# Kernel optimization log

Hardware: AMD Instinct MI355X
Metric: run time of the kernel (lower is better)

Reference implementation:

```python
import jax, jax.numpy as jnp
import numpy as np

B, N, D, M, C = 4, 256, 128, 128, 128


def _lin_init(key, din, dout):
    # torch nn.Linear default: U(-1/sqrt(din), 1/sqrt(din)) for weight and bias
    bound = 1.0 / np.sqrt(din)
    kw, kb = jax.random.split(key)
    W = jax.random.uniform(kw, (din, dout), jnp.float32, -bound, bound)
    b = jax.random.uniform(kb, (dout,), jnp.float32, -bound, bound)
    return W, b


def setup_inputs() -> dict:
    key = jax.random.key(0)
    k_h, k_adj, k1, k2, k3, k4 = jax.random.split(key, 6)
    h = jax.random.normal(k_h, (B, N, D), jnp.float32)
    adj = jax.random.uniform(k_adj, (B, N, N), jnp.float32)
    # msg MLP: Linear(2D -> M), SiLU, Linear(M -> M). Split first weight into
    # the h_i block (W1a) and h_j block (W1b) of the concatenated input.
    W1, b1 = _lin_init(k1, 2 * D, M)
    W1a, W1b = W1[:D], W1[D:]
    W2, b2 = _lin_init(k2, M, M)
    # to_c MLP: Linear(M -> M), SiLU, Linear(M -> C)
    Wc1, bc1 = _lin_init(k3, M, M)
    Wc2, bc2 = _lin_init(k4, M, C)
    return {"h": h, "adj": adj, "W1a": W1a, "W1b": W1b, "b1": b1,
            "W2": W2, "b2": b2, "Wc1": Wc1, "bc1": bc1, "Wc2": Wc2, "bc2": bc2}


def reference(h, adj, W1a, W1b, b1, W2, b2, Wc1, bc1, Wc2, bc2):
    n = h.shape[1]
    # First msg Linear on cat([h_i, h_j]) == h_i @ W1a + h_j @ W1b + b1.
    # Precompute per-node projections once instead of the (B,N,N,2D) pair tensor.
    pi = jnp.einsum('bnd,dm->bnm', h, W1a)           # (B,N,M) for destination i
    pj = jnp.einsum('bnd,dm->bnm', h, W1b)           # (B,N,M) for source j
    pre = pi[:, :, None, :] + pj[:, None, :, :] + b1  # (B,N,N,M)
    m = jnp.einsum('bijm,mk->bijk', jax.nn.silu(pre), W2) + b2  # (B,N,N,M)
    # zero self-messages (diagonal ignored), then weight by adjacency
    mask = (1.0 - jnp.eye(n, dtype=h.dtype))[None, :, :, None]
    m = m * mask * adj[..., None]
    # mean aggregation over source nodes j with clamped degree
    denom = jnp.clip(jnp.sum(adj, axis=-1, keepdims=True), 1.0)  # (B,N,1)
    m_agg = jnp.sum(m, axis=2) / denom                           # (B,N,M)
    c = jnp.einsum('bnm,mc->bnc', jax.nn.silu(jnp.einsum('bnm,mk->bnk', m_agg, Wc1) + bc1), Wc2) + bc2
    return c
```

## Files before the change

### kernel.cpp

```cpp
#include <hip/hip_runtime.h>
#include <math.h>

#define BB 4
#define NN 256
#define DD 128
#define MM 128
#define CC 128
#define ROWS (BB * NN)

static __device__ __forceinline__ float fast_exp2(float x) {
#if __has_builtin(__builtin_amdgcn_exp2f)
    return __builtin_amdgcn_exp2f(x);
#else
    return __exp2f(x);
#endif
}

static __device__ __forceinline__ float fast_rcp(float x) {
#if __has_builtin(__builtin_amdgcn_rcpf)
    return __builtin_amdgcn_rcpf(x);
#else
    return 1.0f / x;
#endif
}

static __device__ __forceinline__ float silu_f(float x) {
    float e = fast_exp2(-1.44269504088896340736f * x);
    return x * fast_rcp(1.0f + e);
}

template <int R>
__global__ __launch_bounds__(256) void k_proj(const float* __restrict__ h,
                                              const float* __restrict__ W1a,
                                              const float* __restrict__ W1b,
                                              const float* __restrict__ b1,
                                              float* __restrict__ pibias,
                                              float* __restrict__ pj) {
    __shared__ float sWa[32 * MM];
    __shared__ float sWb[32 * MM];
    __shared__ float sH[R * DD];

    const int t = threadIdx.x;
    const int m = t & 127;
    const int rh = t >> 7;
    const int row0 = blockIdx.x * R;

    const float bias = b1[m];

    const float* hbase = h + (size_t)row0 * DD;
    sH[t] = hbase[t];
    sH[t + 256] = hbase[t + 256];

    float accA[2] = {0.0f, 0.0f};
    float accB[2] = {0.0f, 0.0f};

    for (int c = 0; c < 4; ++c) {
        __syncthreads();
        const float4* ga = (const float4*)(W1a + (size_t)c * 32 * MM);
        const float4* gb = (const float4*)(W1b + (size_t)c * 32 * MM);
        float4* la = (float4*)sWa;
        float4* lb = (float4*)sWb;
        #pragma unroll
        for (int i = 0; i < 4; ++i) {
            la[t + 256 * i] = ga[t + 256 * i];
            lb[t + 256 * i] = gb[t + 256 * i];
        }
        __syncthreads();

        #pragma unroll 8
        for (int dd = 0; dd < 32; ++dd) {
            const int d = c * 32 + dd;
            const float wa = sWa[dd * MM + m];
            const float wb = sWb[dd * MM + m];
            #pragma unroll
            for (int r = 0; r < 2; ++r) {
                const float hv = sH[(rh * 2 + r) * DD + d];
                accA[r] = fmaf(hv, wa, accA[r]);
                accB[r] = fmaf(hv, wb, accB[r]);
            }
        }
    }

    #pragma unroll
    for (int r = 0; r < 2; ++r) {
        const int row = row0 + rh * 2 + r;
        pibias[(size_t)row * MM + m] = accA[r] + bias;
        pj[(size_t)row * MM + m]     = accB[r];
    }
}

__global__ __launch_bounds__(256) void k_msg(const float* __restrict__ adj,
                                             const float* __restrict__ pibias,
                                             const float* __restrict__ pj,
                                             float* __restrict__ S,
                                             float* __restrict__ beta) {
    __shared__ float sPJ[64 * MM];
    __shared__ float sAdj[2][NN];
    __shared__ float sRed[2][256];
    __shared__ float sWred[2][4];

    const int t = threadIdx.x;
    const int pairIdx = blockIdx.x;
    const int b = pairIdx >> 7;
    const int i0 = (pairIdx & 127) * 2;
    const int row0 = b * NN + i0;

    const int m = t & 127;
    const int jh = t >> 7;

    const float* arow = adj + (size_t)row0 * NN;
    const float a0v = arow[t];
    const float a1v = arow[t + 256];
    const float pim0 = pibias[(size_t)row0 * MM + m];
    const float pim1 = pibias[(size_t)(row0 + 1) * MM + m];

    sAdj[0][t] = a0v;
    sAdj[1][t] = a1v;
    __syncthreads();

    float v0 = a0v, v1 = a1v;
    #pragma unroll
    for (int off = 32; off > 0; off >>= 1) {
        v0 += __shfl_xor(v0, off, 64);
        v1 += __shfl_xor(v1, off, 64);
    }
    if ((t & 63) == 0) { sWred[0][t >> 6] = v0; sWred[1][t >> 6] = v1; }
    __syncthreads();
    const float A0 = sWred[0][0] + sWred[0][1] + sWred[0][2] + sWred[0][3];
    const float A1 = sWred[1][0] + sWred[1][1] + sWred[1][2] + sWred[1][3];
    const float aii0 = sAdj[0][i0];
    const float aii1 = sAdj[1][i0 + 1];
    __syncthreads();
    if (t == 0) { sAdj[0][i0] = 0.0f; sAdj[1][i0 + 1] = 0.0f; }

    const float inv0 = 1.0f / fmaxf(A0, 1.0f);
    const float inv1 = 1.0f / fmaxf(A1, 1.0f);

    const float* __restrict__ pjB = pj + (size_t)b * NN * MM;

    float acc0 = 0.0f, acc1 = 0.0f;
    for (int c = 0; c < 4; ++c) {
        __syncthreads();
        const float4* g = (const float4*)(pjB + (size_t)c * 64 * MM);
        float4* l = (float4*)sPJ;
        #pragma unroll
        for (int i = 0; i < 8; ++i) l[t + 256 * i] = g[t + 256 * i];
        __syncthreads();

        #pragma unroll 8
        for (int jj = jh; jj < 64; jj += 2) {
            const int j = c * 64 + jj;
            const float pjv = sPJ[jj * MM + m];
            const float w0 = sAdj[0][j];
            const float w1 = sAdj[1][j];
            acc0 = fmaf(w0, silu_f(pim0 + pjv), acc0);
            acc1 = fmaf(w1, silu_f(pim1 + pjv), acc1);
        }
    }

    sRed[0][t] = acc0;
    sRed[1][t] = acc1;
    __syncthreads();
    if (t < 128) {
        S[(size_t)row0 * MM + t] = (sRed[0][t] + sRed[0][t + 128]) * inv0;
    } else {
        const int k = t - 128;
        S[(size_t)(row0 + 1) * MM + k] = (sRed[1][k] + sRed[1][k + 128]) * inv1;
    }
    if (t == 0) {
        beta[row0]     = (A0 - aii0) * inv0;
        beta[row0 + 1] = (A1 - aii1) * inv1;
    }
}

__device__ __forceinline__ void matvec_staged(const float* __restrict__ W,
                                              const float* __restrict__ src,
                                              float* __restrict__ sW,
                                              float acc[2], int t, int k, int rh) {
    for (int c = 0; c < 2; ++c) {
        __syncthreads();
        const float4* g = (const float4*)(W + (size_t)c * 64 * MM);
        float4* l = (float4*)sW;
        #pragma unroll
        for (int i = 0; i < 8; ++i) l[t + 256 * i] = g[t + 256 * i];
        __syncthreads();

        #pragma unroll 8
        for (int dd = 0; dd < 64; ++dd) {
            const int d = c * 64 + dd;
            const float wv = sW[dd * MM + k];
            acc[0] = fmaf(src[(rh * 2 + 0) * MM + d], wv, acc[0]);
            acc[1] = fmaf(src[(rh * 2 + 1) * MM + d], wv, acc[1]);
        }
    }
}

template <int R>
__global__ __launch_bounds__(256) void k_out(const float* __restrict__ S,
                                             const float* __restrict__ beta,
                                             const float* __restrict__ W2,
                                             const float* __restrict__ b2,
                                             const float* __restrict__ Wc1,
                                             const float* __restrict__ bc1,
                                             const float* __restrict__ Wc2,
                                             const float* __restrict__ bc2,
                                             float* __restrict__ out) {
    __shared__ float sW[64 * MM];
    __shared__ float sA[R * MM];
    __shared__ float sB[R * MM];

    const int t = threadIdx.x;
    const int k = t & 127;
    const int rh = t >> 7;
    const int row0 = blockIdx.x * R;

    const float bet0 = beta[row0 + rh * 2];
    const float bet1 = beta[row0 + rh * 2 + 1];
    const float b2k  = b2[k];
    const float bc1k = bc1[k];
    const float bc2k = bc2[k];

    const float* sbase = S + (size_t)row0 * MM;
    sA[t] = sbase[t];
    sA[t + 256] = sbase[t + 256];

    float acc[2];

    acc[0] = bet0 * b2k;
    acc[1] = bet1 * b2k;
    matvec_staged(W2, sA, sW, acc, t, k, rh);
    sB[(rh * 2 + 0) * MM + k] = acc[0];
    sB[(rh * 2 + 1) * MM + k] = acc[1];

    acc[0] = bc1k;
    acc[1] = bc1k;
    matvec_staged(Wc1, sB, sW, acc, t, k, rh);
    sA[(rh * 2 + 0) * MM + k] = silu_f(acc[0]);
    sA[(rh * 2 + 1) * MM + k] = silu_f(acc[1]);

    acc[0] = bc2k;
    acc[1] = bc2k;
    matvec_staged(Wc2, sA, sW, acc, t, k, rh);
    out[(size_t)(row0 + rh * 2 + 0) * CC + k] = acc[0];
    out[(size_t)(row0 + rh * 2 + 1) * CC + k] = acc[1];
}

extern "C" void kernel_launch(void* const* d_in, const int* in_sizes, int n_in,
                              void* d_out, int out_size, void* d_ws, size_t ws_size,
                              hipStream_t stream) {
    const float* h   = (const float*)d_in[0];
    const float* adj = (const float*)d_in[1];
    const float* W1a = (const float*)d_in[2];
    const float* W1b = (const float*)d_in[3];
    const float* b1  = (const float*)d_in[4];
    const float* W2  = (const float*)d_in[5];
    const float* b2  = (const float*)d_in[6];
    const float* Wc1 = (const float*)d_in[7];
    const float* bc1 = (const float*)d_in[8];
    const float* Wc2 = (const float*)d_in[9];
    const float* bc2 = (const float*)d_in[10];
    float* out = (float*)d_out;

    float* ws = (float*)d_ws;
    float* pibias = ws;
    float* pj     = ws + (size_t)ROWS * MM;
    float* S      = ws + (size_t)2 * ROWS * MM;
    float* beta   = ws + (size_t)3 * ROWS * MM;

    k_proj<4><<<ROWS / 4, 256, 0, stream>>>(h, W1a, W1b, b1, pibias, pj);
    k_msg<<<ROWS / 2, 256, 0, stream>>>(adj, pibias, pj, S, beta);
    k_out<4><<<ROWS / 4, 256, 0, stream>>>(S, beta, W2, b2, Wc1, bc1, Wc2, bc2, out);
}
```

Baseline: 105.8 us.

## Fuse three kernels into one cooperative kernel with grid sync

Replaces the projection, message and output kernels with a single cooperative kernel of 256 blocks, each handling 4 rows. A grid-wide sync separates the projection phase from the message phase, and only pj goes through global memory. pibias, S and beta stay in shared memory. Each block now processes 4 destination rows per pj pass instead of 2, halving pj re-staging, and the final MLP matvecs split the reduction dimension across the two thread halves. In exchange there are fewer blocks (256 on a GPU with many CUs), the cost of a grid sync, and larger shared memory use, which lowers parallelism in the dominant message phase.

```diff
diff --git a/kernel.cpp b/kernel.cpp
--- a/kernel.cpp
+++ b/kernel.cpp
@@ -1,5 +1,8 @@
 #include <hip/hip_runtime.h>
+#include <hip/hip_cooperative_groups.h>
 #include <math.h>
+
+namespace cg = cooperative_groups;
 
 #define BB 4
 #define NN 256
@@ -29,154 +32,11 @@
     return x * fast_rcp(1.0f + e);
 }
 
-template <int R>
-__global__ __launch_bounds__(256) void k_proj(const float* __restrict__ h,
-                                              const float* __restrict__ W1a,
-                                              const float* __restrict__ W1b,
-                                              const float* __restrict__ b1,
-                                              float* __restrict__ pibias,
-                                              float* __restrict__ pj) {
-    __shared__ float sWa[32 * MM];
-    __shared__ float sWb[32 * MM];
-    __shared__ float sH[R * DD];
-
-    const int t = threadIdx.x;
-    const int m = t & 127;
-    const int rh = t >> 7;
-    const int row0 = blockIdx.x * R;
-
-    const float bias = b1[m];
-
-    const float* hbase = h + (size_t)row0 * DD;
-    sH[t] = hbase[t];
-    sH[t + 256] = hbase[t + 256];
-
-    float accA[2] = {0.0f, 0.0f};
-    float accB[2] = {0.0f, 0.0f};
-
-    for (int c = 0; c < 4; ++c) {
-        __syncthreads();
-        const float4* ga = (const float4*)(W1a + (size_t)c * 32 * MM);
-        const float4* gb = (const float4*)(W1b + (size_t)c * 32 * MM);
-        float4* la = (float4*)sWa;
-        float4* lb = (float4*)sWb;
-        #pragma unroll
-        for (int i = 0; i < 4; ++i) {
-            la[t + 256 * i] = ga[t + 256 * i];
-            lb[t + 256 * i] = gb[t + 256 * i];
-        }
-        __syncthreads();
-
-        #pragma unroll 8
-        for (int dd = 0; dd < 32; ++dd) {
-            const int d = c * 32 + dd;
-            const float wa = sWa[dd * MM + m];
-            const float wb = sWb[dd * MM + m];
-            #pragma unroll
-            for (int r = 0; r < 2; ++r) {
-                const float hv = sH[(rh * 2 + r) * DD + d];
-                accA[r] = fmaf(hv, wa, accA[r]);
-                accB[r] = fmaf(hv, wb, accB[r]);
-            }
-        }
-    }
-
-    #pragma unroll
-    for (int r = 0; r < 2; ++r) {
-        const int row = row0 + rh * 2 + r;
-        pibias[(size_t)row * MM + m] = accA[r] + bias;
-        pj[(size_t)row * MM + m]     = accB[r];
-    }
-}
-
-__global__ __launch_bounds__(256) void k_msg(const float* __restrict__ adj,
-                                             const float* __restrict__ pibias,
-                                             const float* __restrict__ pj,
-                                             float* __restrict__ S,
-                                             float* __restrict__ beta) {
-    __shared__ float sPJ[64 * MM];
-    __shared__ float sAdj[2][NN];
-    __shared__ float sRed[2][256];
-    __shared__ float sWred[2][4];
-
-    const int t = threadIdx.x;
-    const int pairIdx = blockIdx.x;
-    const int b = pairIdx >> 7;
-    const int i0 = (pairIdx & 127) * 2;
-    const int row0 = b * NN + i0;
-
-    const int m = t & 127;
-    const int jh = t >> 7;
-
-    const float* arow = adj + (size_t)row0 * NN;
-    const float a0v = arow[t];
-    const float a1v = arow[t + 256];
-    const float pim0 = pibias[(size_t)row0 * MM + m];
-    const float pim1 = pibias[(size_t)(row0 + 1) * MM + m];
-
-    sAdj[0][t] = a0v;
-    sAdj[1][t] = a1v;
-    __syncthreads();
-
-    float v0 = a0v, v1 = a1v;
-    #pragma unroll
-    for (int off = 32; off > 0; off >>= 1) {
-        v0 += __shfl_xor(v0, off, 64);
-        v1 += __shfl_xor(v1, off, 64);
-    }
-    if ((t & 63) == 0) { sWred[0][t >> 6] = v0; sWred[1][t >> 6] = v1; }
-    __syncthreads();
-    const float A0 = sWred[0][0] + sWred[0][1] + sWred[0][2] + sWred[0][3];
-    const float A1 = sWred[1][0] + sWred[1][1] + sWred[1][2] + sWred[1][3];
-    const float aii0 = sAdj[0][i0];
-    const float aii1 = sAdj[1][i0 + 1];
-    __syncthreads();
-    if (t == 0) { sAdj[0][i0] = 0.0f; sAdj[1][i0 + 1] = 0.0f; }
-
-    const float inv0 = 1.0f / fmaxf(A0, 1.0f);
-    const float inv1 = 1.0f / fmaxf(A1, 1.0f);
-
-    const float* __restrict__ pjB = pj + (size_t)b * NN * MM;
-
-    float acc0 = 0.0f, acc1 = 0.0f;
-    for (int c = 0; c < 4; ++c) {
-        __syncthreads();
-        const float4* g = (const float4*)(pjB + (size_t)c * 64 * MM);
-        float4* l = (float4*)sPJ;
-        #pragma unroll
-        for (int i = 0; i < 8; ++i) l[t + 256 * i] = g[t + 256 * i];
-        __syncthreads();
-
-        #pragma unroll 8
-        for (int jj = jh; jj < 64; jj += 2) {
-            const int j = c * 64 + jj;
-            const float pjv = sPJ[jj * MM + m];
-            const float w0 = sAdj[0][j];
-            const float w1 = sAdj[1][j];
-            acc0 = fmaf(w0, silu_f(pim0 + pjv), acc0);
-            acc1 = fmaf(w1, silu_f(pim1 + pjv), acc1);
-        }
-    }
-
-    sRed[0][t] = acc0;
-    sRed[1][t] = acc1;
-    __syncthreads();
-    if (t < 128) {
-        S[(size_t)row0 * MM + t] = (sRed[0][t] + sRed[0][t + 128]) * inv0;
-    } else {
-        const int k = t - 128;
-        S[(size_t)(row0 + 1) * MM + k] = (sRed[1][k] + sRed[1][k + 128]) * inv1;
-    }
-    if (t == 0) {
-        beta[row0]     = (A0 - aii0) * inv0;
-        beta[row0 + 1] = (A1 - aii1) * inv1;
-    }
-}
-
-__device__ __forceinline__ void matvec_staged(const float* __restrict__ W,
+static __device__ __forceinline__ void mat128(const float* __restrict__ W,
                                               const float* __restrict__ src,
                                               float* __restrict__ sW,
-                                              float acc[2], int t, int k, int rh) {
+                                              float* __restrict__ sP,
+                                              float acc[4], int t, int k, int half) {
     for (int c = 0; c < 2; ++c) {
         __syncthreads();
         const float4* g = (const float4*)(W + (size_t)c * 64 * MM);
@@ -185,64 +45,207 @@
         for (int i = 0; i < 8; ++i) l[t + 256 * i] = g[t + 256 * i];
         __syncthreads();
 
+        const int dd0 = half * 32;
         #pragma unroll 8
-        for (int dd = 0; dd < 64; ++dd) {
+        for (int dd = dd0; dd < dd0 + 32; ++dd) {
             const int d = c * 64 + dd;
             const float wv = sW[dd * MM + k];
-            acc[0] = fmaf(src[(rh * 2 + 0) * MM + d], wv, acc[0]);
-            acc[1] = fmaf(src[(rh * 2 + 1) * MM + d], wv, acc[1]);
-        }
-    }
-}
-
-template <int R>
-__global__ __launch_bounds__(256) void k_out(const float* __restrict__ S,
-                                             const float* __restrict__ beta,
+            #pragma unroll
+            for (int r = 0; r < 4; ++r) acc[r] = fmaf(src[r * MM + d], wv, acc[r]);
+        }
+    }
+    if (half == 1) {
+        #pragma unroll
+        for (int r = 0; r < 4; ++r) sP[r * MM + k] = acc[r];
+    }
+    __syncthreads();
+    if (half == 0) {
+        #pragma unroll
+        for (int r = 0; r < 4; ++r) acc[r] += sP[r * MM + k];
+    }
+}
+
+__global__ __launch_bounds__(256) void fused(const float* __restrict__ h,
+                                             const float* __restrict__ adj,
+                                             const float* __restrict__ W1a,
+                                             const float* __restrict__ W1b,
+                                             const float* __restrict__ b1,
                                              const float* __restrict__ W2,
                                              const float* __restrict__ b2,
                                              const float* __restrict__ Wc1,
                                              const float* __restrict__ bc1,
                                              const float* __restrict__ Wc2,
                                              const float* __restrict__ bc2,
-                                             float* __restrict__ out) {
-    __shared__ float sW[64 * MM];
-    __shared__ float sA[R * MM];
-    __shared__ float sB[R * MM];
+                                             float* __restrict__ out,
+                                             float* __restrict__ pjws) {
+    __shared__ float sStage[64 * MM];
+    __shared__ float sH[4 * DD];
+    __shared__ float sPib[4 * MM];
+    __shared__ float sAdj[4][NN];
+    __shared__ float sRed[4 * 256];
+    __shared__ float sS[4 * MM];
+    __shared__ float sB[4 * MM];
+    __shared__ float sWred[4][4];
 
     const int t = threadIdx.x;
-    const int k = t & 127;
-    const int rh = t >> 7;
-    const int row0 = blockIdx.x * R;
-
-    const float bet0 = beta[row0 + rh * 2];
-    const float bet1 = beta[row0 + rh * 2 + 1];
-    const float b2k  = b2[k];
-    const float bc1k = bc1[k];
-    const float bc2k = bc2[k];
-
-    const float* sbase = S + (size_t)row0 * MM;
-    sA[t] = sbase[t];
-    sA[t + 256] = sbase[t + 256];
-
-    float acc[2];
-
-    acc[0] = bet0 * b2k;
-    acc[1] = bet1 * b2k;
-    matvec_staged(W2, sA, sW, acc, t, k, rh);
-    sB[(rh * 2 + 0) * MM + k] = acc[0];
-    sB[(rh * 2 + 1) * MM + k] = acc[1];
-
-    acc[0] = bc1k;
-    acc[1] = bc1k;
-    matvec_staged(Wc1, sB, sW, acc, t, k, rh);
-    sA[(rh * 2 + 0) * MM + k] = silu_f(acc[0]);
-    sA[(rh * 2 + 1) * MM + k] = silu_f(acc[1]);
-
-    acc[0] = bc2k;
-    acc[1] = bc2k;
-    matvec_staged(Wc2, sA, sW, acc, t, k, rh);
-    out[(size_t)(row0 + rh * 2 + 0) * CC + k] = acc[0];
-    out[(size_t)(row0 + rh * 2 + 1) * CC + k] = acc[1];
+    const int blk = blockIdx.x;
+    const int row0 = blk * 4;
+    const int b = blk >> 6;
+    const int i0 = (blk & 63) * 4;
+
+    const int m = t & 127;
+    const int half = t >> 7;
+
+    const float b1m  = b1[m];
+    const float b2k  = b2[m];
+    const float bc1k = bc1[m];
+    const float bc2k = bc2[m];
+
+    {
+        const float* hbase = h + (size_t)row0 * DD;
+        sH[t] = hbase[t];
+        sH[t + 256] = hbase[t + 256];
+
+        float accA0 = 0.f, accA1 = 0.f, accB0 = 0.f, accB1 = 0.f;
+        for (int c = 0; c < 4; ++c) {
+            __syncthreads();
+            const float4* ga = (const float4*)(W1a + (size_t)c * 32 * MM);
+            const float4* gb = (const float4*)(W1b + (size_t)c * 32 * MM);
+            float4* la = (float4*)sStage;
+            float4* lb = (float4*)(sStage + 32 * MM);
+            #pragma unroll
+            for (int i = 0; i < 4; ++i) {
+                la[t + 256 * i] = ga[t + 256 * i];
+                lb[t + 256 * i] = gb[t + 256 * i];
+            }
+            __syncthreads();
+            #pragma unroll 8
+            for (int dd = 0; dd < 32; ++dd) {
+                const int d = c * 32 + dd;
+                const float wa = sStage[dd * MM + m];
+                const float wb = sStage[32 * MM + dd * MM + m];
+                const float h0 = sH[(half * 2 + 0) * DD + d];
+                const float h1 = sH[(half * 2 + 1) * DD + d];
+                accA0 = fmaf(h0, wa, accA0);
+                accA1 = fmaf(h1, wa, accA1);
+                accB0 = fmaf(h0, wb, accB0);
+                accB1 = fmaf(h1, wb, accB1);
+            }
+        }
+        sPib[(half * 2 + 0) * MM + m] = accA0 + b1m;
+        sPib[(half * 2 + 1) * MM + m] = accA1 + b1m;
+        float* pjrow = pjws + (size_t)(row0 + half * 2) * MM;
+        pjrow[m]      = accB0;
+        pjrow[MM + m] = accB1;
+    }
+
+    cg::this_grid().sync();
+
+    float inv[4], bet[4];
+    {
+        const float* arow = adj + (size_t)row0 * NN;
+        float* sAdjF = (float*)sAdj;
+        #pragma unroll
+        for (int i = 0; i < 4; ++i) sAdjF[t + 256 * i] = arow[t + 256 * i];
+        __syncthreads();
+
+        float v0 = sAdj[0][t], v1 = sAdj[1][t], v2 = sAdj[2][t], v3 = sAdj[3][t];
+        #pragma unroll
+        for (int off = 32; off > 0; off >>= 1) {
+            v0 += __shfl_xor(v0, off, 64);
+            v1 += __shfl_xor(v1, off, 64);
+            v2 += __shfl_xor(v2, off, 64);
+            v3 += __shfl_xor(v3, off, 64);
+        }
+        if ((t & 63) == 0) {
+            const int w = t >> 6;
+            sWred[0][w] = v0; sWred[1][w] = v1; sWred[2][w] = v2; sWred[3][w] = v3;
+        }
+        __syncthreads();
+        float A[4], aii[4];
+        #pragma unroll
+        for (int r = 0; r < 4; ++r) {
+            A[r] = sWred[r][0] + sWred[r][1] + sWred[r][2] + sWred[r][3];
+            aii[r] = sAdj[r][i0 + r];
+        }
+        __syncthreads();
+        if (t < 4) sAdj[t][i0 + t] = 0.0f;
+        #pragma unroll
+        for (int r = 0; r < 4; ++r) {
+            inv[r] = 1.0f / fmaxf(A[r], 1.0f);
+            bet[r] = (A[r] - aii[r]) * inv[r];
+        }
+
+        const float pim0 = sPib[0 * MM + m];
+        const float pim1 = sPib[1 * MM + m];
+        const float pim2 = sPib[2 * MM + m];
+        const float pim3 = sPib[3 * MM + m];
+        const float* __restrict__ pjB = pjws + (size_t)b * NN * MM;
+
+        float acc0 = 0.f, acc1 = 0.f, acc2 = 0.f, acc3 = 0.f;
+        for (int c = 0; c < 4; ++c) {
+            __syncthreads();
+            const float4* g = (const float4*)(pjB + (size_t)c * 64 * MM);
+            float4* l = (float4*)sStage;
+            #pragma unroll
+            for (int i = 0; i < 8; ++i) l[t + 256 * i] = g[t + 256 * i];
+            __syncthreads();
+
+            #pragma unroll 4
+            for (int jj = half; jj < 64; jj += 2) {
+                const int j = c * 64 + jj;
+                const float pjv = sStage[jj * MM + m];
+                const float w0 = sAdj[0][j];
+                const float w1 = sAdj[1][j];
+                const float w2 = sAdj[2][j];
+                const float w3 = sAdj[3][j];
+                acc0 = fmaf(w0, silu_f(pim0 + pjv), acc0);
+                acc1 = fmaf(w1, silu_f(pim1 + pjv), acc1);
+                acc2 = fmaf(w2, silu_f(pim2 + pjv), acc2);
+                acc3 = fmaf(w3, silu_f(pim3 + pjv), acc3);
+            }
+        }
+
+        sRed[0 * 256 + t] = acc0;
+        sRed[1 * 256 + t] = acc1;
+        sRed[2 * 256 + t] = acc2;
+        sRed[3 * 256 + t] = acc3;
+        __syncthreads();
+        if (t < 128) {
+            #pragma unroll
+            for (int r = 0; r < 4; ++r)
+                sS[r * MM + t] = (sRed[r * 256 + t] + sRed[r * 256 + t + 128]) * inv[r];
+        }
+    }
+
+    {
+        float acc[4];
+
+        #pragma unroll
+        for (int r = 0; r < 4; ++r) acc[r] = (half == 0) ? bet[r] * b2k : 0.0f;
+        mat128(W2, sS, sStage, sRed, acc, t, m, half);
+        if (half == 0) {
+            #pragma unroll
+            for (int r = 0; r < 4; ++r) sB[r * MM + m] = acc[r];
+        }
+
+        #pragma unroll
+        for (int r = 0; r < 4; ++r) acc[r] = (half == 0) ? bc1k : 0.0f;
+        mat128(Wc1, sB, sStage, sRed, acc, t, m, half);
+        if (half == 0) {
+            #pragma unroll
+            for (int r = 0; r < 4; ++r) sS[r * MM + m] = silu_f(acc[r]);
+        }
+
+        #pragma unroll
+        for (int r = 0; r < 4; ++r) acc[r] = (half == 0) ? bc2k : 0.0f;
+        mat128(Wc2, sS, sStage, sRed, acc, t, m, half);
+        if (half == 0) {
+            #pragma unroll
+            for (int r = 0; r < 4; ++r)
+                out[(size_t)(row0 + r) * CC + m] = acc[r];
+        }
+    }
 }
 
 extern "C" void kernel_launch(void* const* d_in, const int* in_sizes, int n_in,
@@ -260,14 +263,11 @@
     const float* Wc2 = (const float*)d_in[9];
     const float* bc2 = (const float*)d_in[10];
     float* out = (float*)d_out;
-
-    float* ws = (float*)d_ws;
-    float* pibias = ws;
-    float* pj     = ws + (size_t)ROWS * MM;
-    float* S      = ws + (size_t)2 * ROWS * MM;
-    float* beta   = ws + (size_t)3 * ROWS * MM;
-
-    k_proj<4><<<ROWS / 4, 256, 0, stream>>>(h, W1a, W1b, b1, pibias, pj);
-    k_msg<<<ROWS / 2, 256, 0, stream>>>(adj, pibias, pj, S, beta);
-    k_out<4><<<ROWS / 4, 256, 0, stream>>>(S, beta, W2, b2, Wc1, bc1, Wc2, bc2, out);
-}
+    float* pjws = (float*)d_ws;
+
+    void* args[] = {(void*)&h, (void*)&adj, (void*)&W1a, (void*)&W1b, (void*)&b1,
+                    (void*)&W2, (void*)&b2, (void*)&Wc1, (void*)&bc1,
+                    (void*)&Wc2, (void*)&bc2, (void*)&out, (void*)&pjws};
+    hipLaunchCooperativeKernel(reinterpret_cast<void*>(fused),
+                               dim3(256), dim3(256), args, 0, stream);
+}
```

After: 150.3 us. +42.1%, slower.

## Fuse message aggregation and output MLP into one kernel, shrink projection tiles

Applied to the files above, without the earlier changes.

Merges the message-aggregation kernel with the output MLP kernel so S and beta stay in shared memory instead of going through global memory, and removes one launch. The projection kernel now handles 2 rows per block instead of 4. In exchange, each block stages W2, Wc1 and Wc2 for only two rows, doubling weight reloads from L2 across the grid.

```diff
diff --git a/kernel.cpp b/kernel.cpp
--- a/kernel.cpp
+++ b/kernel.cpp
@@ -29,7 +29,6 @@
     return x * fast_rcp(1.0f + e);
 }
 
-template <int R>
 __global__ __launch_bounds__(256) void k_proj(const float* __restrict__ h,
                                               const float* __restrict__ W1a,
                                               const float* __restrict__ W1b,
@@ -38,22 +37,18 @@
                                               float* __restrict__ pj) {
     __shared__ float sWa[32 * MM];
     __shared__ float sWb[32 * MM];
-    __shared__ float sH[R * DD];
+    __shared__ float sH[2 * DD];
 
     const int t = threadIdx.x;
     const int m = t & 127;
-    const int rh = t >> 7;
-    const int row0 = blockIdx.x * R;
+    const int r = t >> 7;
+    const int row0 = blockIdx.x * 2;
 
     const float bias = b1[m];
 
-    const float* hbase = h + (size_t)row0 * DD;
-    sH[t] = hbase[t];
-    sH[t + 256] = hbase[t + 256];
-
-    float accA[2] = {0.0f, 0.0f};
-    float accB[2] = {0.0f, 0.0f};
-
+    sH[t] = h[(size_t)row0 * DD + t];
+
+    float accA = 0.0f, accB = 0.0f;
     for (int c = 0; c < 4; ++c) {
         __syncthreads();
         const float4* ga = (const float4*)(W1a + (size_t)c * 32 * MM);
@@ -70,50 +65,52 @@
         #pragma unroll 8
         for (int dd = 0; dd < 32; ++dd) {
             const int d = c * 32 + dd;
-            const float wa = sWa[dd * MM + m];
-            const float wb = sWb[dd * MM + m];
-            #pragma unroll
-            for (int r = 0; r < 2; ++r) {
-                const float hv = sH[(rh * 2 + r) * DD + d];
-                accA[r] = fmaf(hv, wa, accA[r]);
-                accB[r] = fmaf(hv, wb, accB[r]);
-            }
-        }
-    }
-
-    #pragma unroll
-    for (int r = 0; r < 2; ++r) {
-        const int row = row0 + rh * 2 + r;
-        pibias[(size_t)row * MM + m] = accA[r] + bias;
-        pj[(size_t)row * MM + m]     = accB[r];
-    }
-}
-
-__global__ __launch_bounds__(256) void k_msg(const float* __restrict__ adj,
-                                             const float* __restrict__ pibias,
-                                             const float* __restrict__ pj,
-                                             float* __restrict__ S,
-                                             float* __restrict__ beta) {
-    __shared__ float sPJ[64 * MM];
+            const float hv = sH[r * DD + d];
+            accA = fmaf(hv, sWa[dd * MM + m], accA);
+            accB = fmaf(hv, sWb[dd * MM + m], accB);
+        }
+    }
+
+    const int row = row0 + r;
+    pibias[(size_t)row * MM + m] = accA + bias;
+    pj[(size_t)row * MM + m]     = accB;
+}
+
+__global__ __launch_bounds__(256) void k_msgout(const float* __restrict__ adj,
+                                                const float* __restrict__ pibias,
+                                                const float* __restrict__ pj,
+                                                const float* __restrict__ W2,
+                                                const float* __restrict__ b2,
+                                                const float* __restrict__ Wc1,
+                                                const float* __restrict__ bc1,
+                                                const float* __restrict__ Wc2,
+                                                const float* __restrict__ bc2,
+                                                float* __restrict__ out) {
+    __shared__ float sStage[64 * MM];
     __shared__ float sAdj[2][NN];
     __shared__ float sRed[2][256];
+    __shared__ float sS[2 * MM];
+    __shared__ float sB[2 * MM];
     __shared__ float sWred[2][4];
 
     const int t = threadIdx.x;
-    const int pairIdx = blockIdx.x;
-    const int b = pairIdx >> 7;
-    const int i0 = (pairIdx & 127) * 2;
+    const int blk = blockIdx.x;
+    const int b = blk >> 7;
+    const int i0 = (blk & 127) * 2;
     const int row0 = b * NN + i0;
 
     const int m = t & 127;
-    const int jh = t >> 7;
+    const int half = t >> 7;
+
+    const float b2k  = b2[m];
+    const float bc1k = bc1[m];
+    const float bc2k = bc2[m];
+    const float pim0 = pibias[(size_t)row0 * MM + m];
+    const float pim1 = pibias[(size_t)(row0 + 1) * MM + m];
 
     const float* arow = adj + (size_t)row0 * NN;
     const float a0v = arow[t];
     const float a1v = arow[t + 256];
-    const float pim0 = pibias[(size_t)row0 * MM + m];
-    const float pim1 = pibias[(size_t)(row0 + 1) * MM + m];
-
     sAdj[0][t] = a0v;
     sAdj[1][t] = a1v;
     __syncthreads();
@@ -135,22 +132,23 @@
 
     const float inv0 = 1.0f / fmaxf(A0, 1.0f);
     const float inv1 = 1.0f / fmaxf(A1, 1.0f);
+    const float bet0 = (A0 - aii0) * inv0;
+    const float bet1 = (A1 - aii1) * inv1;
 
     const float* __restrict__ pjB = pj + (size_t)b * NN * MM;
-
     float acc0 = 0.0f, acc1 = 0.0f;
     for (int c = 0; c < 4; ++c) {
         __syncthreads();
         const float4* g = (const float4*)(pjB + (size_t)c * 64 * MM);
-        float4* l = (float4*)sPJ;
-        #pragma unroll
-        for (int i = 0; i < 8; ++i) l[t + 256 * i] = g[t + 256 * i];
-        __syncthreads();
-
-        #pragma unroll 8
-        for (int jj = jh; jj < 64; jj += 2) {
+        float4* l = (float4*)sStage;
+        #pragma unroll
+        for (int i = 0; i < 8; ++i) l[t + 256 * i] = g[t + 256 * i];
+        __syncthreads();
+
+        #pragma unroll 8
+        for (int jj = half; jj < 64; jj += 2) {
             const int j = c * 64 + jj;
-            const float pjv = sPJ[jj * MM + m];
+            const float pjv = sStage[jj * MM + m];
             const float w0 = sAdj[0][j];
             const float w1 = sAdj[1][j];
             acc0 = fmaf(w0, silu_f(pim0 + pjv), acc0);
@@ -162,87 +160,62 @@
     sRed[1][t] = acc1;
     __syncthreads();
     if (t < 128) {
-        S[(size_t)row0 * MM + t] = (sRed[0][t] + sRed[0][t + 128]) * inv0;
+        sS[t] = (sRed[0][t] + sRed[0][t + 128]) * inv0;
     } else {
         const int k = t - 128;
-        S[(size_t)(row0 + 1) * MM + k] = (sRed[1][k] + sRed[1][k + 128]) * inv1;
-    }
-    if (t == 0) {
-        beta[row0]     = (A0 - aii0) * inv0;
-        beta[row0 + 1] = (A1 - aii1) * inv1;
-    }
-}
-
-__device__ __forceinline__ void matvec_staged(const float* __restrict__ W,
-                                              const float* __restrict__ src,
-                                              float* __restrict__ sW,
-                                              float acc[2], int t, int k, int rh) {
+        sS[MM + k] = (sRed[1][k] + sRed[1][k + 128]) * inv1;
+    }
+
+    const float betr = (half == 0) ? bet0 : bet1;
+
+    float acc = betr * b2k;
     for (int c = 0; c < 2; ++c) {
         __syncthreads();
-        const float4* g = (const float4*)(W + (size_t)c * 64 * MM);
-        float4* l = (float4*)sW;
-        #pragma unroll
-        for (int i = 0; i < 8; ++i) l[t + 256 * i] = g[t + 256 * i];
-        __syncthreads();
-
+        const float4* g = (const float4*)(W2 + (size_t)c * 64 * MM);
+        float4* l = (float4*)sStage;
+        #pragma unroll
+        for (int i = 0; i < 8; ++i) l[t + 256 * i] = g[t + 256 * i];
+        __syncthreads();
         #pragma unroll 8
         for (int dd = 0; dd < 64; ++dd) {
             const int d = c * 64 + dd;
-            const float wv = sW[dd * MM + k];
-            acc[0] = fmaf(src[(rh * 2 + 0) * MM + d], wv, acc[0]);
-            acc[1] = fmaf(src[(rh * 2 + 1) * MM + d], wv, acc[1]);
-        }
-    }
-}
-
-template <int R>
-__global__ __launch_bounds__(256) void k_out(const float* __restrict__ S,
-                                             const float* __restrict__ beta,
-                                             const float* __restrict__ W2,
-                                             const float* __restrict__ b2,
-                                             const float* __restrict__ Wc1,
-                                             const float* __restrict__ bc1,
-                                             const float* __restrict__ Wc2,
-                                             const float* __restrict__ bc2,
-                                             float* __restrict__ out) {
-    __shared__ float sW[64 * MM];
-    __shared__ float sA[R * MM];
-    __shared__ float sB[R * MM];
-
-    const int t = threadIdx.x;
-    const int k = t & 127;
-    const int rh = t >> 7;
-    const int row0 = blockIdx.x * R;
-
-    const float bet0 = beta[row0 + rh * 2];
-    const float bet1 = beta[row0 + rh * 2 + 1];
-    const float b2k  = b2[k];
-    const float bc1k = bc1[k];
-    const float bc2k = bc2[k];
-
-    const float* sbase = S + (size_t)row0 * MM;
-    sA[t] = sbase[t];
-    sA[t + 256] = sbase[t + 256];
-
-    float acc[2];
-
-    acc[0] = bet0 * b2k;
-    acc[1] = bet1 * b2k;
-    matvec_staged(W2, sA, sW, acc, t, k, rh);
-    sB[(rh * 2 + 0) * MM + k] = acc[0];
-    sB[(rh * 2 + 1) * MM + k] = acc[1];
-
-    acc[0] = bc1k;
-    acc[1] = bc1k;
-    matvec_staged(Wc1, sB, sW, acc, t, k, rh);
-    sA[(rh * 2 + 0) * MM + k] = silu_f(acc[0]);
-    sA[(rh * 2 + 1) * MM + k] = silu_f(acc[1]);
-
-    acc[0] = bc2k;
-    acc[1] = bc2k;
-    matvec_staged(Wc2, sA, sW, acc, t, k, rh);
-    out[(size_t)(row0 + rh * 2 + 0) * CC + k] = acc[0];
-    out[(size_t)(row0 + rh * 2 + 1) * CC + k] = acc[1];
+            acc = fmaf(sS[half * MM + d], sStage[dd * MM + m], acc);
+        }
+    }
+    sB[half * MM + m] = acc;
+
+    acc = bc1k;
+    for (int c = 0; c < 2; ++c) {
+        __syncthreads();
+        const float4* g = (const float4*)(Wc1 + (size_t)c * 64 * MM);
+        float4* l = (float4*)sStage;
+        #pragma unroll
+        for (int i = 0; i < 8; ++i) l[t + 256 * i] = g[t + 256 * i];
+        __syncthreads();
+        #pragma unroll 8
+        for (int dd = 0; dd < 64; ++dd) {
+            const int d = c * 64 + dd;
+            acc = fmaf(sB[half * MM + d], sStage[dd * MM + m], acc);
+        }
+    }
+    __syncthreads();
+    sS[half * MM + m] = silu_f(acc);
+
+    acc = bc2k;
+    for (int c = 0; c < 2; ++c) {
+        __syncthreads();
+        const float4* g = (const float4*)(Wc2 + (size_t)c * 64 * MM);
+        float4* l = (float4*)sStage;
+        #pragma unroll
+        for (int i = 0; i < 8; ++i) l[t + 256 * i] = g[t + 256 * i];
+        __syncthreads();
+        #pragma unroll 8
+        for (int dd = 0; dd < 64; ++dd) {
+            const int d = c * 64 + dd;
+            acc = fmaf(sS[half * MM + d], sStage[dd * MM + m], acc);
+        }
+    }
+    out[(size_t)(row0 + half) * CC + m] = acc;
 }
 
 extern "C" void kernel_launch(void* const* d_in, const int* in_sizes, int n_in,
@@ -264,10 +237,8 @@
     float* ws = (float*)d_ws;
     float* pibias = ws;
     float* pj     = ws + (size_t)ROWS * MM;
-    float* S      = ws + (size_t)2 * ROWS * MM;
-    float* beta   = ws + (size_t)3 * ROWS * MM;
-
-    k_proj<4><<<ROWS / 4, 256, 0, stream>>>(h, W1a, W1b, b1, pibias, pj);
-    k_msg<<<ROWS / 2, 256, 0, stream>>>(adj, pibias, pj, S, beta);
-    k_out<4><<<ROWS / 4, 256, 0, stream>>>(S, beta, W2, b2, Wc1, bc1, Wc2, bc2, out);
-}
+
+    k_proj<<<ROWS / 2, 256, 0, stream>>>(h, W1a, W1b, b1, pibias, pj);
+    k_msgout<<<ROWS / 2, 256, 0, stream>>>(adj, pibias, pj, W2, b2, Wc1, bc1,
+                                           Wc2, bc2, out);
+}
```

Measured after the change: 102.0 us. 1.04x faster.
